# Kernel tuning notes

Measured on AMD Instinct MI355X. Metric: run time of the kernel, lower is better.

## Reference

```python
import jax, jax.numpy as jnp
import numpy as np

N, NFEAT, NHID, NCLASS, NHEADS = 8192, 512, 64, 16, 4
ALPHA = 0.2          # leaky_relu slope for attention scores
OUT_SLOPE = 0.01     # flax default slope for per-head output leaky_relu
NEG = -9000000000000000.0


def glorot(key, shape):
    fan_in, fan_out = shape[0], shape[1]
    lim = jnp.sqrt(6.0 / (fan_in + fan_out))
    return jax.random.uniform(key, shape, jnp.float32, -lim, lim)


def setup_inputs() -> dict:
    key = jax.random.key(0)
    ks = jax.random.split(key, 6)
    x = jax.random.normal(ks[0], (N, NFEAT), jnp.float32)
    adj = jax.random.randint(ks[1], (N, N), 0, 2, jnp.int32)
    Wh = glorot(ks[2], (NHEADS * NFEAT, NHID)).reshape(NHEADS, NFEAT, NHID)
    ah = glorot(ks[3], (NHEADS * 2 * NHID, 1)).reshape(NHEADS, 2 * NHID, 1)
    Wo = glorot(ks[4], (NHID * NHEADS, NCLASS))
    ao = glorot(ks[5], (2 * NCLASS, 1))
    return {"x": x, "adj": adj, "Wh": Wh, "ah": ah, "Wo": Wo, "ao": ao}


def _gat_layer(x, adj_mask, W, a, score_slope):
    # h: (N, F)
    h = x @ W
    F = h.shape[1]
    # a_input[i,j] = concat(h_i, h_j); a_input @ a == f1[i] + f2[j]
    f1 = h @ a[:F, 0]   # (N,)
    f2 = h @ a[F:, 0]   # (N,)
    e = jax.nn.leaky_relu(f1[:, None] + f2[None, :], negative_slope=score_slope)
    att = jax.nn.softmax(jnp.where(adj_mask, e, NEG), axis=1)  # (N, N)
    return att @ h  # (N, F)


def reference(x, adj, Wh, ah, Wo, ao):
    adj_mask = adj > 0
    heads = []
    for k in range(NHEADS):  # small fixed structural loop
        hp = _gat_layer(x, adj_mask, Wh[k], ah[k], ALPHA)
        heads.append(jax.nn.leaky_relu(hp, negative_slope=OUT_SLOPE))
    xcat = jnp.concatenate(heads, axis=1)  # (N, NHEADS*NHID)
    # output head: concat=False -> return h_prime directly
    return _gat_layer(xcat, adj_mask, Wo, ao, ALPHA)  # (N, NCLASS)
```

## Files before the change

kernel.cpp:

```cpp
#include <hip/hip_runtime.h>
#include <stdint.h>

#define N      8192
#define NW32   256
#define FEAT   512
#define HID    64
#define NH     4
#define C1     256
#define PCH    65
#define TC     260
#define NCLS   16
#define C2     32
#define IPB    8
#define LOG2E  1.44269504f

typedef __attribute__((ext_vector_type(8))) short bf16x8;
typedef __attribute__((ext_vector_type(4))) float f32x4;

__device__ __forceinline__ float b2f(uint16_t u){
  uint32_t x = ((uint32_t)u) << 16;
  return __builtin_bit_cast(float, x);
}
__device__ __forceinline__ uint16_t f2b(float f){
  uint32_t x = __builtin_bit_cast(uint32_t, f);
  uint32_t r = (x + 0x7fffu + ((x >> 16) & 1u)) >> 16;
  return (uint16_t)r;
}
__device__ __forceinline__ float lrelu(float v, float a){ return fmaxf(v, a * v); }
__device__ __forceinline__ float fexp2(float x){
#if __has_builtin(__builtin_amdgcn_exp2f)
  return __builtin_amdgcn_exp2f(x);
#else
  return exp2f(x);
#endif
}
__device__ __forceinline__ uint32_t pk_bf16(float lo, float hi){
  uint32_t r;
  asm("v_cvt_pk_bf16_f32 %0, %1, %2" : "=v"(r) : "v"(lo), "v"(hi));
  return r;
}

__device__ __forceinline__ bf16x8 mk_frag(float f1v, float4 fa, float4 fb,
                                          uint32_t ub, float& dsum){
  float e0, e1, e2, e3, e4, e5, e6, e7, s;
  s = f1v + fa.x; e0 = fexp2(fmaxf(s, 0.2f * s)); if (!(ub &   1u)) e0 = 0.f;
  s = f1v + fa.y; e1 = fexp2(fmaxf(s, 0.2f * s)); if (!(ub &   2u)) e1 = 0.f;
  s = f1v + fa.z; e2 = fexp2(fmaxf(s, 0.2f * s)); if (!(ub &   4u)) e2 = 0.f;
  s = f1v + fa.w; e3 = fexp2(fmaxf(s, 0.2f * s)); if (!(ub &   8u)) e3 = 0.f;
  s = f1v + fb.x; e4 = fexp2(fmaxf(s, 0.2f * s)); if (!(ub &  16u)) e4 = 0.f;
  s = f1v + fb.y; e5 = fexp2(fmaxf(s, 0.2f * s)); if (!(ub &  32u)) e5 = 0.f;
  s = f1v + fb.z; e6 = fexp2(fmaxf(s, 0.2f * s)); if (!(ub &  64u)) e6 = 0.f;
  s = f1v + fb.w; e7 = fexp2(fmaxf(s, 0.2f * s)); if (!(ub & 128u)) e7 = 0.f;
  dsum += ((e0 + e1) + (e2 + e3)) + ((e4 + e5) + (e6 + e7));
  union { uint32_t u[4]; bf16x8 v; } r;
  r.u[0] = pk_bf16(e0, e1);
  r.u[1] = pk_bf16(e2, e3);
  r.u[2] = pk_bf16(e4, e5);
  r.u[3] = pk_bf16(e6, e7);
  return r.v;
}

__global__ __launch_bounds__(256) void kp_pack(const int* __restrict__ adj,
                                               unsigned long long* __restrict__ adjP64){
  int t = threadIdx.x;
  int lane = t & 63;
  int wg = blockIdx.x * 4 + (t >> 6);
  for (int it = 0; it < 128; ++it){
    size_t c = (size_t)it * 8192 + wg;
    int v = adj[c * 64 + lane];
    unsigned long long m = __ballot(v > 0);
    if (lane == 0) adjP64[c] = m;
  }
}

__global__ void k0_wht(const float* __restrict__ Wh, float* __restrict__ WhT){
  int idx = blockIdx.x * 256 + threadIdx.x;
  int k = idx >> 15;
  int r = idx & 32767;
  int cc = r >> 9, f = r & 511;
  WhT[idx] = Wh[k * 32768 + f * 64 + cc];
}

__global__ __launch_bounds__(256) void k1_h(const float* __restrict__ x,
    const float* __restrict__ WhT, const float* __restrict__ ah,
    uint16_t* __restrict__ H, float* __restrict__ f1, float* __restrict__ f2)
{
  __shared__ float4 xs[IPB][128];
  int t = threadIdx.x;
  int i0 = blockIdx.x * IPB;
  for (int r = t; r < IPB * 128; r += 256){
    int ii = r >> 7, o = r & 127;
    xs[ii][o] = *((const float4*)(x + (size_t)(i0 + ii) * FEAT) + o);
  }
  __syncthreads();
  int k = t >> 6, cc = t & 63;
  const float4* wrow = (const float4*)(WhT + k * 32768 + cc * 512);
  float acc[IPB] = {};
  for (int f4 = 0; f4 < 128; ++f4){
    float4 wv = wrow[f4];
    #pragma unroll
    for (int ii = 0; ii < IPB; ++ii){
      float4 xv = xs[ii][f4];
      acc[ii] += xv.x * wv.x + xv.y * wv.y + xv.z * wv.z + xv.w * wv.w;
    }
  }
  float a1 = ah[k * 128 + cc], a2 = ah[k * 128 + 64 + cc];
  #pragma unroll
  for (int ii = 0; ii < IPB; ++ii){
    int i = i0 + ii;
    H[(size_t)i * C1 + t] = f2b(acc[ii]);
    float c1v = acc[ii] * a1, c2v = acc[ii] * a2;
    #pragma unroll
    for (int off = 32; off; off >>= 1){
      c1v += __shfl_down(c1v, off);
      c2v += __shfl_down(c2v, off);
    }
    if (cc == 0){ f1[k * N + i] = c1v * LOG2E; f2[k * N + i] = c2v * LOG2E; }
  }
}

__global__ void k2a_htT(const uint16_t* __restrict__ H, uint16_t* __restrict__ HT){
  __shared__ uint16_t tile[64][65];
  int bid = blockIdx.x;
  int k = bid & 3, it = bid >> 2;
  int i0 = it * 64;
  int t = threadIdx.x;
  #pragma unroll
  for (int r = 0; r < 4; ++r){
    int ii = r * 16 + (t >> 4);
    int pp = (t & 15) * 4;
    uint2 v = *(const uint2*)(H + (size_t)(i0 + ii) * C1 + k * 64 + pp);
    const uint16_t* s = (const uint16_t*)&v;
    tile[pp + 0][ii] = s[0]; tile[pp + 1][ii] = s[1];
    tile[pp + 2][ii] = s[2]; tile[pp + 3][ii] = s[3];
  }
  __syncthreads();
  #pragma unroll
  for (int r = 0; r < 4; ++r){
    int pp = r * 16 + (t >> 4);
    int ii = (t & 15) * 4;
    uint2 v;
    uint16_t* s = (uint16_t*)&v;
    s[0] = tile[pp][ii + 0]; s[1] = tile[pp][ii + 1];
    s[2] = tile[pp][ii + 2]; s[3] = tile[pp][ii + 3];
    *(uint2*)(HT + (size_t)k * (64 * N) + (size_t)pp * N + i0 + ii) = v;
  }
}

#define K3_BODY(JC, CUR, NXT)                                                   \
  {                                                                             \
    *(uint4*)&Hl[(JC) & 1][p0][o40 * 8] = h##CUR##0;                            \
    *(uint4*)&Hl[(JC) & 1][p1][o40 * 8] = h##CUR##1;                            \
    const int gjn = js * 2048 + (((JC) + 1) & 63) * 32;                         \
    h##NXT##0 = *(const uint4*)(src0 + gjn);                                    \
    h##NXT##1 = *(const uint4*)(src1 + gjn);                                    \
    w##NXT##0 = adjP[arow0 + (gjn >> 5)];                                       \
    w##NXT##1 = adjP[arow1 + (gjn >> 5)];                                       \
    f##NXT##0 = *(const float4*)(f2h + gjn + 8 * q);                            \
    f##NXT##1 = *(const float4*)(f2h + gjn + 8 * q + 4);                        \
    bf16x8 af0 = mk_frag(f1v0, f##CUR##0, f##CUR##1,                            \
                         (w##CUR##0 >> (8 * q)) & 255u, dsum0);                 \
    bf16x8 af1 = mk_frag(f1v1, f##CUR##0, f##CUR##1,                            \
                         (w##CUR##1 >> (8 * q)) & 255u, dsum1);                 \
    __syncthreads();                                                            \
    _Pragma("unroll")                                                           \
    for (int ct = 0; ct < 4; ++ct){                                             \
      bf16x8 bfr = *(const bf16x8*)&Hl[(JC) & 1][head * 64 + ct * 16 + m][q * 8]; \
      acc[0][ct] = __builtin_amdgcn_mfma_f32_16x16x32_bf16(af0, bfr, acc[0][ct], 0, 0, 0); \
      acc[1][ct] = __builtin_amdgcn_mfma_f32_16x16x32_bf16(af1, bfr, acc[1][ct], 0, 0, 0); \
    }                                                                           \
  }

__global__ __launch_bounds__(512, 4) void k3_attA(const uint32_t* __restrict__ adjP,
    const uint16_t* __restrict__ HT, const float* __restrict__ f1,
    const float* __restrict__ f2, float* __restrict__ accA)
{
  __shared__ uint16_t Hl[2][256][40];

  const int t = threadIdx.x;
  const int ibl = blockIdx.x >> 2;
  const int js = blockIdx.x & 3;
  const int gi0 = ibl * 64;

  const int lane = t & 63;
  const int w    = t >> 6;
  const int head = w >> 1;
  const int ith  = w & 1;
  const int m    = lane & 15;
  const int q    = lane >> 4;

  const int p0 = t >> 2, o40 = t & 3;
  const int p1 = p0 + 128;
  const uint16_t* src0 = HT + (size_t)p0 * N + o40 * 8;
  const uint16_t* src1 = HT + (size_t)p1 * N + o40 * 8;

  const int row0 = gi0 + ith * 32 + m;
  const int arow0 = row0 * NW32;
  const int arow1 = (row0 + 16) * NW32;
  const float* f2h = f2 + (size_t)head * N;
  const float f1v0 = f1[(size_t)head * N + row0];
  const float f1v1 = f1[(size_t)head * N + row0 + 16];

  f32x4 acc[2][4] = {};
  float dsum0 = 0.f, dsum1 = 0.f;

  uint4 hA0, hA1, hB0, hB1;
  uint32_t wA0, wA1, wB0, wB1;
  float4 fA0, fA1, fB0, fB1;

  {
    const int gj0 = js * 2048;
    hA0 = *(const uint4*)(src0 + gj0);
    hA1 = *(const uint4*)(src1 + gj0);
    wA0 = adjP[arow0 + (gj0 >> 5)];
    wA1 = adjP[arow1 + (gj0 >> 5)];
    fA0 = *(const float4*)(f2h + gj0 + 8 * q);
    fA1 = *(const float4*)(f2h + gj0 + 8 * q + 4);
  }

  for (int jc = 0; jc < 64; jc += 2){
    K3_BODY(jc,     A, B)
    K3_BODY(jc + 1, B, A)
  }

  #pragma unroll
  for (int itl = 0; itl < 2; ++itl)
    #pragma unroll
    for (int ct = 0; ct < 4; ++ct)
      #pragma unroll
      for (int reg = 0; reg < 4; ++reg){
        int gi = gi0 + ith * 32 + itl * 16 + q * 4 + reg;
        accA[((size_t)js * N + gi) * TC + head * PCH + ct * 16 + m] = acc[itl][ct][reg];
      }
  {
    float v0 = dsum0, v1 = dsum1;
    v0 += __shfl_xor(v0, 16); v0 += __shfl_xor(v0, 32);
    v1 += __shfl_xor(v1, 16); v1 += __shfl_xor(v1, 32);
    if (q == 0){
      accA[((size_t)js * N + row0)      * TC + head * PCH + 64] = v0;
      accA[((size_t)js * N + row0 + 16) * TC + head * PCH + 64] = v1;
    }
  }
}

__global__ void k4_redA(const float* __restrict__ accA, uint16_t* __restrict__ xcat){
  int i = blockIdx.x;
  int t = threadIdx.x;
  int k = t >> 6, cc = t & 63;
  size_t base = (size_t)i * TC + k * PCH;
  float v = 0.f, Z = 0.f;
  #pragma unroll
  for (int js = 0; js < 4; ++js){
    const float* p = accA + (size_t)js * N * TC + base;
    v += p[cc];
    Z += p[64];
  }
  float r = v / Z;
  xcat[(size_t)i * C1 + t] = f2b(lrelu(r, 0.01f));
}

__global__ __launch_bounds__(256) void k5_h2(const uint16_t* __restrict__ xcat,
    const float* __restrict__ Wo, const float* __restrict__ ao,
    uint16_t* __restrict__ h2T, float* __restrict__ f1o, float* __restrict__ f2o)
{
  __shared__ uint16_t xs[16][256];
  int t = threadIdx.x;
  int i0 = blockIdx.x * 16;
  #pragma unroll
  for (int r = 0; r < 2; ++r){
    int idx = t + 256 * r;
    int ii = idx >> 5, o4 = idx & 31;
    *(uint4*)&xs[ii][o4 * 8] = *(const uint4*)(xcat + (size_t)(i0 + ii) * C1 + o4 * 8);
  }
  __syncthreads();
  int ii = t >> 4, c = t & 15;
  float acc = 0.f;
  for (int f = 0; f < 256; ++f)
    acc += b2f(xs[ii][f]) * Wo[f * 16 + c];
  int i = i0 + ii;
  h2T[(size_t)c * N + i] = f2b(acc);
  float u1 = acc * ao[c];
  float u2 = acc * ao[16 + c];
  #pragma unroll
  for (int off = 8; off; off >>= 1){
    u1 += __shfl_down(u1, off, 16);
    u2 += __shfl_down(u2, off, 16);
  }
  if (c == 0){ f1o[i] = u1 * LOG2E; f2o[i] = u2 * LOG2E; }
}

#define K6_BODY(JC, CUR, NXT)                                                   \
  {                                                                             \
    if (stg) *(uint4*)&Hl[(JC) & 1][p0][o40 * 8] = h##CUR;                      \
    const int gjn = js * 1024 + (((JC) + 1) & 31) * 32;                         \
    if (stg) h##NXT = *(const uint4*)(h2T + (size_t)p0 * N + gjn + o40 * 8);    \
    w##NXT = adjP[arow + (gjn >> 5)];                                           \
    f##NXT##0 = *(const float4*)(f2o + gjn + 8 * q);                            \
    f##NXT##1 = *(const float4*)(f2o + gjn + 8 * q + 4);                        \
    bf16x8 af = mk_frag(f1v, f##CUR##0, f##CUR##1,                              \
                        (w##CUR >> (8 * q)) & 255u, dsum);                      \
    __syncthreads();                                                            \
    bf16x8 b0 = *(const bf16x8*)&Hl[(JC) & 1][m][q * 8];                        \
    acc0 = __builtin_amdgcn_mfma_f32_16x16x32_bf16(af, b0, acc0, 0, 0, 0);      \
  }

__global__ __launch_bounds__(256) void k6_attB(const uint32_t* __restrict__ adjP,
    const uint16_t* __restrict__ h2T, const float* __restrict__ f1o,
    const float* __restrict__ f2o, float* __restrict__ accB)
{
  __shared__ uint16_t Hl[2][16][40];

  const int t = threadIdx.x;
  const int ibl = blockIdx.x >> 3;
  const int js = blockIdx.x & 7;
  const int gi0 = ibl * 64;

  const int lane = t & 63;
  const int w = t >> 6;
  const int m = lane & 15;
  const int q = lane >> 4;

  const int p0 = t >> 2, o40 = t & 3;
  const bool stg = (t < 64);

  const int row = gi0 + w * 16 + m;
  const int arow = row * NW32;
  const float f1v = f1o[row];

  f32x4 acc0 = {0.f, 0.f, 0.f, 0.f};
  float dsum = 0.f;

  uint4 hA = {}, hB = {};
  uint32_t wA, wB;
  float4 fA0, fA1, fB0, fB1;

  {
    const int gj0 = js * 1024;
    if (stg) hA = *(const uint4*)(h2T + (size_t)p0 * N + gj0 + o40 * 8);
    wA = adjP[arow + (gj0 >> 5)];
    fA0 = *(const float4*)(f2o + gj0 + 8 * q);
    fA1 = *(const float4*)(f2o + gj0 + 8 * q + 4);
  }

  for (int jc = 0; jc < 32; jc += 2){
    K6_BODY(jc,     A, B)
    K6_BODY(jc + 1, B, A)
  }

  #pragma unroll
  for (int reg = 0; reg < 4; ++reg){
    int gi = gi0 + w * 16 + q * 4 + reg;
    accB[((size_t)js * N + gi) * C2 + m] = acc0[reg];
  }
  {
    float v = dsum;
    v += __shfl_xor(v, 16); v += __shfl_xor(v, 32);
    if (q == 0)
      accB[((size_t)js * N + row) * C2 + 16] = v;
  }
}

__global__ void k7_redB(const float* __restrict__ accB, float* __restrict__ out){
  int idx = blockIdx.x * 256 + threadIdx.x;
  int i = idx >> 4, c = idx & 15;
  float v = 0.f, Z = 0.f;
  #pragma unroll
  for (int js = 0; js < 8; ++js){
    const float* p = accB + ((size_t)js * N + i) * C2;
    v += p[c];
    Z += p[16];
  }
  out[idx] = v / Z;
}

extern "C" void kernel_launch(void* const* d_in, const int* in_sizes, int n_in,
                              void* d_out, int out_size, void* d_ws, size_t ws_size,
                              hipStream_t stream)
{
  const float* x   = (const float*)d_in[0];
  const int*   adj = (const int*)d_in[1];
  const float* Wh  = (const float*)d_in[2];
  const float* ah  = (const float*)d_in[3];
  const float* Wo  = (const float*)d_in[4];
  const float* ao  = (const float*)d_in[5];
  float* out = (float*)d_out;

  char* ws = (char*)d_ws;
  float*    WhT  = (float*)   (ws);
  uint16_t* H    = (uint16_t*)(ws + 524288);
  uint16_t* HT   = (uint16_t*)(ws + 4718592);
  float*    f1   = (float*)   (ws + 8912896);
  float*    f2   = (float*)   (ws + 9043968);
  float*    accA = (float*)   (ws + 9175040);
  uint16_t* xcat = (uint16_t*)(ws + 43253760);
  uint16_t* h2T  = (uint16_t*)(ws + 47448064);
  float*    f1o  = (float*)   (ws + 47710208);
  float*    f2o  = (float*)   (ws + 47742976);
  float*    accB = (float*)   (ws + 47775744);
  void*     adjP = (void*)    (ws + 56164352);

  hipLaunchKernelGGL(kp_pack,  dim3(2048), dim3(256), 0, stream, adj, (unsigned long long*)adjP);
  hipLaunchKernelGGL(k0_wht,   dim3(512),  dim3(256), 0, stream, Wh, WhT);
  hipLaunchKernelGGL(k1_h,     dim3(1024), dim3(256), 0, stream, x, WhT, ah, H, f1, f2);
  hipLaunchKernelGGL(k2a_htT,  dim3(512),  dim3(256), 0, stream, H, HT);
  hipLaunchKernelGGL(k3_attA,  dim3(512),  dim3(512), 0, stream, (const uint32_t*)adjP, HT, f1, f2, accA);
  hipLaunchKernelGGL(k4_redA,  dim3(8192), dim3(256), 0, stream, accA, xcat);
  hipLaunchKernelGGL(k5_h2,    dim3(512),  dim3(256), 0, stream, xcat, Wo, ao, h2T, f1o, f2o);
  hipLaunchKernelGGL(k6_attB,  dim3(1024), dim3(256), 0, stream, (const uint32_t*)adjP, h2T, f1o, f2o, accB);
  hipLaunchKernelGGL(k7_redB,  dim3(512),  dim3(256), 0, stream, accB, out);
}
```

Baseline: 615.1 us.

## Load attention B-fragments directly from global memory, drop LDS staging and barriers

Both attention kernels now have each lane load its MFMA B operand (bf16x8 of transposed H) straight from global memory into registers. This removes the shared-memory double buffer and the per-chunk __syncthreads. k3 is reshaped to 256-thread blocks of 32 rows with one head per wave, and block indexing is reordered so the j-split is the slow dimension, which may improve L2 reuse of H tiles. The trade-off is redundant global loads of H across waves and blocks in place of cooperative staging, plus more registers for the prefetched fragments.

Measured after the change: 716.6 us. 1.16x slower.

```diff
diff --git a/kernel.cpp b/kernel.cpp
--- a/kernel.cpp
+++ b/kernel.cpp
@@ -149,11 +149,10 @@
 
 #define K3_BODY(JC, CUR, NXT)                                                   \
   {                                                                             \
-    *(uint4*)&Hl[(JC) & 1][p0][o40 * 8] = h##CUR##0;                            \
-    *(uint4*)&Hl[(JC) & 1][p1][o40 * 8] = h##CUR##1;                            \
     const int gjn = js * 2048 + (((JC) + 1) & 63) * 32;                         \
-    h##NXT##0 = *(const uint4*)(src0 + gjn);                                    \
-    h##NXT##1 = *(const uint4*)(src1 + gjn);                                    \
+    _Pragma("unroll")                                                           \
+    for (int ct = 0; ct < 4; ++ct)                                              \
+      b##NXT[ct] = *(const bf16x8*)(hbase + (size_t)ct * 16 * N + gjn);         \
     w##NXT##0 = adjP[arow0 + (gjn >> 5)];                                       \
     w##NXT##1 = adjP[arow1 + (gjn >> 5)];                                       \
     f##NXT##0 = *(const float4*)(f2h + gjn + 8 * q);                            \
@@ -162,56 +161,47 @@
                          (w##CUR##0 >> (8 * q)) & 255u, dsum0);                 \
     bf16x8 af1 = mk_frag(f1v1, f##CUR##0, f##CUR##1,                            \
                          (w##CUR##1 >> (8 * q)) & 255u, dsum1);                 \
-    __syncthreads();                                                            \
     _Pragma("unroll")                                                           \
     for (int ct = 0; ct < 4; ++ct){                                             \
-      bf16x8 bfr = *(const bf16x8*)&Hl[(JC) & 1][head * 64 + ct * 16 + m][q * 8]; \
-      acc[0][ct] = __builtin_amdgcn_mfma_f32_16x16x32_bf16(af0, bfr, acc[0][ct], 0, 0, 0); \
-      acc[1][ct] = __builtin_amdgcn_mfma_f32_16x16x32_bf16(af1, bfr, acc[1][ct], 0, 0, 0); \
+      acc[0][ct] = __builtin_amdgcn_mfma_f32_16x16x32_bf16(af0, b##CUR[ct], acc[0][ct], 0, 0, 0); \
+      acc[1][ct] = __builtin_amdgcn_mfma_f32_16x16x32_bf16(af1, b##CUR[ct], acc[1][ct], 0, 0, 0); \
     }                                                                           \
   }
 
-__global__ __launch_bounds__(512, 4) void k3_attA(const uint32_t* __restrict__ adjP,
+__global__ __launch_bounds__(256, 4) void k3_attA(const uint32_t* __restrict__ adjP,
     const uint16_t* __restrict__ HT, const float* __restrict__ f1,
     const float* __restrict__ f2, float* __restrict__ accA)
 {
-  __shared__ uint16_t Hl[2][256][40];
-
   const int t = threadIdx.x;
-  const int ibl = blockIdx.x >> 2;
-  const int js = blockIdx.x & 3;
-  const int gi0 = ibl * 64;
+  const int ibl = blockIdx.x & 255;
+  const int js  = blockIdx.x >> 8;
+  const int gi0 = ibl * 32;
 
   const int lane = t & 63;
-  const int w    = t >> 6;
-  const int head = w >> 1;
-  const int ith  = w & 1;
+  const int head = t >> 6;
   const int m    = lane & 15;
   const int q    = lane >> 4;
 
-  const int p0 = t >> 2, o40 = t & 3;
-  const int p1 = p0 + 128;
-  const uint16_t* src0 = HT + (size_t)p0 * N + o40 * 8;
-  const uint16_t* src1 = HT + (size_t)p1 * N + o40 * 8;
-
-  const int row0 = gi0 + ith * 32 + m;
+  const int row0  = gi0 + m;
   const int arow0 = row0 * NW32;
   const int arow1 = (row0 + 16) * NW32;
   const float* f2h = f2 + (size_t)head * N;
   const float f1v0 = f1[(size_t)head * N + row0];
   const float f1v1 = f1[(size_t)head * N + row0 + 16];
+  const uint16_t* hbase = HT + (size_t)(head * 64 + m) * N + 8 * q;
 
   f32x4 acc[2][4] = {};
   float dsum0 = 0.f, dsum1 = 0.f;
 
-  uint4 hA0, hA1, hB0, hB1;
+  bf16x8 bA[4], bB[4];
   uint32_t wA0, wA1, wB0, wB1;
   float4 fA0, fA1, fB0, fB1;
 
   {
     const int gj0 = js * 2048;
-    hA0 = *(const uint4*)(src0 + gj0);
-    hA1 = *(const uint4*)(src1 + gj0);
+    #pragma unroll
+    for (int ct = 0; ct < 4; ++ct)
+      bA[ct] = *(const bf16x8*)(hbase + (size_t)ct * 16 * N + gj0);
     wA0 = adjP[arow0 + (gj0 >> 5)];
     wA1 = adjP[arow1 + (gj0 >> 5)];
     fA0 = *(const float4*)(f2h + gj0 + 8 * q);
@@ -229,7 +219,7 @@
     for (int ct = 0; ct < 4; ++ct)
       #pragma unroll
       for (int reg = 0; reg < 4; ++reg){
-        int gi = gi0 + ith * 32 + itl * 16 + q * 4 + reg;
+        int gi = gi0 + itl * 16 + q * 4 + reg;
         accA[((size_t)js * N + gi) * TC + head * PCH + ct * 16 + m] = acc[itl][ct][reg];
       }
   {
@@ -291,28 +281,23 @@
 
 #define K6_BODY(JC, CUR, NXT)                                                   \
   {                                                                             \
-    if (stg) *(uint4*)&Hl[(JC) & 1][p0][o40 * 8] = h##CUR;                      \
     const int gjn = js * 1024 + (((JC) + 1) & 31) * 32;                         \
-    if (stg) h##NXT = *(const uint4*)(h2T + (size_t)p0 * N + gjn + o40 * 8);    \
+    b##NXT = *(const bf16x8*)(hbase + gjn);                                     \
     w##NXT = adjP[arow + (gjn >> 5)];                                           \
     f##NXT##0 = *(const float4*)(f2o + gjn + 8 * q);                            \
     f##NXT##1 = *(const float4*)(f2o + gjn + 8 * q + 4);                        \
     bf16x8 af = mk_frag(f1v, f##CUR##0, f##CUR##1,                              \
                         (w##CUR >> (8 * q)) & 255u, dsum);                      \
-    __syncthreads();                                                            \
-    bf16x8 b0 = *(const bf16x8*)&Hl[(JC) & 1][m][q * 8];                        \
-    acc0 = __builtin_amdgcn_mfma_f32_16x16x32_bf16(af, b0, acc0, 0, 0, 0);      \
-  }
-
-__global__ __launch_bounds__(256) void k6_attB(const uint32_t* __restrict__ adjP,
+    acc0 = __builtin_amdgcn_mfma_f32_16x16x32_bf16(af, b##CUR, acc0, 0, 0, 0);  \
+  }
+
+__global__ __launch_bounds__(256, 4) void k6_attB(const uint32_t* __restrict__ adjP,
     const uint16_t* __restrict__ h2T, const float* __restrict__ f1o,
     const float* __restrict__ f2o, float* __restrict__ accB)
 {
-  __shared__ uint16_t Hl[2][16][40];
-
   const int t = threadIdx.x;
-  const int ibl = blockIdx.x >> 3;
-  const int js = blockIdx.x & 7;
+  const int ibl = blockIdx.x & 127;
+  const int js  = blockIdx.x >> 7;
   const int gi0 = ibl * 64;
 
   const int lane = t & 63;
@@ -320,23 +305,21 @@
   const int m = lane & 15;
   const int q = lane >> 4;
 
-  const int p0 = t >> 2, o40 = t & 3;
-  const bool stg = (t < 64);
-
   const int row = gi0 + w * 16 + m;
   const int arow = row * NW32;
   const float f1v = f1o[row];
+  const uint16_t* hbase = h2T + (size_t)m * N + 8 * q;
 
   f32x4 acc0 = {0.f, 0.f, 0.f, 0.f};
   float dsum = 0.f;
 
-  uint4 hA = {}, hB = {};
+  bf16x8 bA, bB;
   uint32_t wA, wB;
   float4 fA0, fA1, fB0, fB1;
 
   {
     const int gj0 = js * 1024;
-    if (stg) hA = *(const uint4*)(h2T + (size_t)p0 * N + gj0 + o40 * 8);
+    bA = *(const bf16x8*)(hbase + gj0);
     wA = adjP[arow + (gj0 >> 5)];
     fA0 = *(const float4*)(f2o + gj0 + 8 * q);
     fA1 = *(const float4*)(f2o + gj0 + 8 * q + 4);
@@ -403,7 +386,7 @@
   hipLaunchKernelGGL(k0_wht,   dim3(512),  dim3(256), 0, stream, Wh, WhT);
   hipLaunchKernelGGL(k1_h,     dim3(1024), dim3(256), 0, stream, x, WhT, ah, H, f1, f2);
   hipLaunchKernelGGL(k2a_htT,  dim3(512),  dim3(256), 0, stream, H, HT);
-  hipLaunchKernelGGL(k3_attA,  dim3(512),  dim3(512), 0, stream, (const uint32_t*)adjP, HT, f1, f2, accA);
+  hipLaunchKernelGGL(k3_attA,  dim3(1024), dim3(256), 0, stream, (const uint32_t*)adjP, HT, f1, f2, accA);
   hipLaunchKernelGGL(k4_redA,  dim3(8192), dim3(256), 0, stream, accA, xcat);
   hipLaunchKernelGGL(k5_h2,    dim3(512),  dim3(256), 0, stream, xcat, Wo, ao, h2T, f1o, f2o);
   hipLaunchKernelGGL(k6_attB,  dim3(1024), dim3(256), 0, stream, (const uint32_t*)adjP, h2T, f1o, f2o, accB);
```
